# Performance work log

Measured on AMD Instinct MI355X. Metric: run time of the kernel, lower is better.

## Reference

```python
import jax, jax.numpy as jnp
import numpy as np

NUM_FUTURE = 4  # num_future_time_steps module constant


def _wmean(x, src, dst, ew, n):
    # Weighted mean aggregation over incoming edges (PyG SAGEConv aggr='mean'
    # with edge-weighted messages). x: [N,F] or [T,N,F].
    if x.ndim == 2:
        msg = x[src] * ew[:, None]                          # [E,F]
        agg = jax.ops.segment_sum(msg, dst, num_segments=n)  # [N,F]
    else:
        msg = x[:, src, :] * ew[None, :, None]              # [T,E,F]
        agg = jax.ops.segment_sum(jnp.moveaxis(msg, 1, 0), dst, num_segments=n)
        agg = jnp.moveaxis(agg, 0, 1)                       # [T,N,F]
    deg = jax.ops.segment_sum(jnp.ones_like(ew), dst, num_segments=n)
    return agg / jnp.clip(deg, 1.0)[:, None]


def _sage(x, src, dst, ew, Wr, Wroot, b, n):
    # WeightedSAGEConv: lin_rel(weighted-mean of neighbors) + lin_root(x)
    return _wmean(x, src, dst, ew, n) @ Wr + x @ Wroot + b


def _glstm(xseq, src, dst, ew, Wr, Wroot, b, h0, c0, n):
    # Graph LSTM: all four gates are WeightedSAGEConv([x_t, h]) ; the gate
    # convs share one gather/scatter (linear in agg), weights stacked to 4H.
    def step(carry, xt):
        h, c = carry
        inp = jnp.concatenate([xt, h], axis=-1)             # [N,2H]
        gates = _wmean(inp, src, dst, ew, n) @ Wr + inp @ Wroot + b  # [N,4H]
        i, f, g, o = jnp.split(gates, 4, axis=-1)
        c = jax.nn.sigmoid(f) * c + jax.nn.sigmoid(i) * jnp.tanh(g)
        h = jax.nn.sigmoid(o) * jnp.tanh(c)
        return (h, c), h
    (h, c), hs = jax.lax.scan(step, (h0, c0), xseq)
    return hs, c  # hs: [T,N,H]


def setup_inputs():
    T, N, E = 12, 20000, 400000
    F, H, O = 32, 64, 8
    key = jax.random.key(0)
    ks = jax.random.split(key, 12)
    nrm = lambda k, shp, fan: jax.random.normal(k, shp, dtype=jnp.float32) / np.float32(np.sqrt(fan))
    return {
        "x": jax.random.normal(ks[0], (T, N, F), dtype=jnp.float32),
        "edge_index": jax.random.randint(ks[1], (2, E), 0, N, dtype=jnp.int32),
        "edge_attr": jax.random.uniform(ks[2], (E,), dtype=jnp.float32),
        "sage_Wr": nrm(ks[3], (F, H), F),
        "sage_Wroot": nrm(ks[4], (F, H), F),
        "sage_b": jnp.zeros((H,), jnp.float32),
        "lstm1_Wr": nrm(ks[5], (2 * H, 4 * H), 2 * H),
        "lstm1_Wroot": nrm(ks[6], (2 * H, 4 * H), 2 * H),
        "lstm1_b": jnp.zeros((4 * H,), jnp.float32),
        "lstm2_Wr": nrm(ks[7], (2 * H, 4 * H), 2 * H),
        "lstm2_Wroot": nrm(ks[8], (2 * H, 4 * H), 2 * H),
        "lstm2_b": jnp.zeros((4 * H,), jnp.float32),
        "W_out": nrm(ks[9], (2 * H, O), 2 * H),
        "b_out": jnp.zeros((O,), jnp.float32),
    }


def reference(x, edge_index, edge_attr, sage_Wr, sage_Wroot, sage_b,
              lstm1_Wr, lstm1_Wroot, lstm1_b, lstm2_Wr, lstm2_Wroot, lstm2_b,
              W_out, b_out):
    src, dst = edge_index[0], edge_index[1]
    N = x.shape[1]
    H = sage_Wr.shape[1]
    emb = _sage(x, src, dst, edge_attr, sage_Wr, sage_Wroot, sage_b, N)  # [T,N,H]
    xr = jax.nn.relu(emb)  # dropout = identity (eval mode)
    h0 = jnp.zeros((N, H), x.dtype)
    c0 = jnp.zeros((N, H), x.dtype)
    h1, c1 = _glstm(xr, src, dst, edge_attr, lstm1_Wr, lstm1_Wroot, lstm1_b, h0, c0, N)
    h2, c2 = _glstm(xr, src, dst, edge_attr, lstm2_Wr, lstm2_Wroot, lstm2_b, h1[-1], c1, N)
    xs = jnp.concatenate([xr, h2], axis=-1)              # skip connection, [T,N,2H]
    out = xs[-NUM_FUTURE:] @ W_out + b_out               # [4,N,O]
    return out, c2, emb
```

## Files before the change

### kernel.cpp

```cpp
#include <hip/hip_runtime.h>
#include <math.h>

#define TT 12
#define FF 32
#define HH 64
#define OO 8
#define GG 256
#define NF 4
#define BR 16

typedef __bf16 bf16x8 __attribute__((ext_vector_type(8)));
typedef float  f32x4  __attribute__((ext_vector_type(4)));

__device__ __forceinline__ float sigmoidf_(float x){ return 1.f/(1.f+expf(-x)); }
__device__ __forceinline__ unsigned short f2bf(float f){
  unsigned int u = __float_as_uint(f);
  u += 0x7FFFu + ((u >> 16) & 1u);
  return (unsigned short)(u >> 16);
}
__device__ __forceinline__ float bf2f(unsigned short b){
  return __uint_as_float(((unsigned int)b) << 16);
}

__global__ void hist_kernel(const int* __restrict__ dst, int* __restrict__ cnt, int E){
  int e = blockIdx.x*blockDim.x + threadIdx.x;
  if (e < E) atomicAdd(&cnt[dst[e]], 1);
}

__global__ __launch_bounds__(1024) void scan_kernel(const int* __restrict__ cnt,
                                                    int* __restrict__ ptr,
                                                    float* __restrict__ invd, int N){
  __shared__ int buf[1024];
  __shared__ int carry;
  if (threadIdx.x == 0) carry = 0;
  __syncthreads();
  for (int base = 0; base < N; base += 1024){
    int i = base + threadIdx.x;
    int v = (i < N) ? cnt[i] : 0;
    buf[threadIdx.x] = v;
    __syncthreads();
    for (int off = 1; off < 1024; off <<= 1){
      int t = (threadIdx.x >= off) ? buf[threadIdx.x - off] : 0;
      __syncthreads();
      buf[threadIdx.x] += t;
      __syncthreads();
    }
    int incl = buf[threadIdx.x];
    if (i < N){
      ptr[i] = carry + incl - v;
      invd[i] = 1.f / fmaxf((float)v, 1.f);
    }
    __syncthreads();
    if (threadIdx.x == 1023){
      carry += incl;
      if (base + 1024 >= N) ptr[N] = carry;
    }
    __syncthreads();
  }
}

__global__ void fill_kernel(const int* __restrict__ src, const int* __restrict__ dst,
                            const float* __restrict__ ew, const int* __restrict__ ptr,
                            int* __restrict__ fill, int2* __restrict__ csr_sw, int E){
  int e = blockIdx.x*blockDim.x + threadIdx.x;
  if (e >= E) return;
  int d = dst[e];
  int pos = ptr[d] + atomicAdd(&fill[d], 1);
  int2 m; m.x = src[e]; m.y = __float_as_int(ew[e]);
  csr_sw[pos] = m;
}

__global__ void bf16_conv(const float* __restrict__ in, unsigned short* __restrict__ out, int n){
  int i = blockIdx.x*blockDim.x + threadIdx.x;
  if (i < n) out[i] = f2bf(in[i]);
}

__global__ void pack_wfrag(const float* __restrict__ Wr, const float* __restrict__ Wroot,
                           unsigned short* __restrict__ Wfrag){
  int idx = blockIdx.x*256 + threadIdx.x;
  if (idx >= 16*8*64*8) return;
  int e  = idx & 7;
  int l  = (idx >> 3) & 63;
  int ks = (idx >> 9) & 7;
  int jt = idx >> 12;
  int k = ks*32 + (l>>4)*8 + e;
  int j = jt*16 + (l&15);
  float v = (k < 128) ? Wr[(size_t)k*GG + j] : Wroot[(size_t)(k-128)*GG + j];
  Wfrag[idx] = f2bf(v);
}

__global__ void pack_sfrag(const float* __restrict__ Wr, const float* __restrict__ Wroot,
                           unsigned short* __restrict__ Sfrag){
  int idx = blockIdx.x*256 + threadIdx.x;
  if (idx >= 4*2*64*8) return;
  int e  = idx & 7;
  int l  = (idx >> 3) & 63;
  int ks = (idx >> 9) & 1;
  int jt = idx >> 10;
  int k = ks*32 + (l>>4)*8 + e;
  int j = jt*16 + (l&15);
  float v = (k < 32) ? Wr[(size_t)k*HH + j] : Wroot[(size_t)(k-32)*HH + j];
  Sfrag[idx] = f2bf(v);
}

__global__ __launch_bounds__(256) void sage_gather(
    const unsigned short* __restrict__ xb, const int* __restrict__ ptr,
    const int2* __restrict__ csr_sw,
    const float* __restrict__ invd, unsigned short* __restrict__ aggb, int N){
  int wave = threadIdx.x >> 6, lane = threadIdx.x & 63;
  int f = lane & 31, tp = lane >> 5;
  int n = blockIdx.x*4 + wave;
  if (n >= N) return;
  int beg = ptr[n], end = ptr[n+1];
  float id = invd[n];
  float acc[TT/2];
  #pragma unroll
  for (int th = 0; th < TT/2; ++th) acc[th] = 0.f;
  const size_t plane = (size_t)N*FF;
  int e = beg;
  for (; e+4 <= end; e += 4){
    int2 m0 = csr_sw[e], m1 = csr_sw[e+1], m2 = csr_sw[e+2], m3 = csr_sw[e+3];
    const unsigned short* p0 = xb + (size_t)m0.x*FF + f + (size_t)tp*plane;
    const unsigned short* p1 = xb + (size_t)m1.x*FF + f + (size_t)tp*plane;
    const unsigned short* p2 = xb + (size_t)m2.x*FF + f + (size_t)tp*plane;
    const unsigned short* p3 = xb + (size_t)m3.x*FF + f + (size_t)tp*plane;
    float w0 = __int_as_float(m0.y), w1 = __int_as_float(m1.y);
    float w2 = __int_as_float(m2.y), w3 = __int_as_float(m3.y);
    #pragma unroll
    for (int th = 0; th < TT/2; ++th)
      acc[th] += bf2f(p0[2*th*plane])*w0 + bf2f(p1[2*th*plane])*w1
               + bf2f(p2[2*th*plane])*w2 + bf2f(p3[2*th*plane])*w3;
  }
  for (; e < end; ++e){
    int2 m = csr_sw[e];
    const unsigned short* p = xb + (size_t)m.x*FF + f + (size_t)tp*plane;
    float wv = __int_as_float(m.y);
    #pragma unroll
    for (int th = 0; th < TT/2; ++th)
      acc[th] += bf2f(p[2*th*plane])*wv;
  }
  #pragma unroll
  for (int th = 0; th < TT/2; ++th)
    aggb[(size_t)(2*th+tp)*plane + (size_t)n*FF + f] = f2bf(acc[th] * id);
}

__global__ __launch_bounds__(256) void sage_mfma(
    const unsigned short* __restrict__ aggb, const unsigned short* __restrict__ xb,
    const unsigned short* __restrict__ Sfrag, const float* __restrict__ bias,
    float* __restrict__ emb, unsigned short* __restrict__ xrb, int Mrows){
  int tid = threadIdx.x, wave = tid >> 6, lane = tid & 63;
  int rbase = blockIdx.x*64 + wave*16;
  if (rbase >= Mrows) return;
  int l15 = lane & 15, l4 = lane >> 4;
  int row = rbase + l15;
  bf16x8 af0 = *(const bf16x8*)&aggb[(size_t)row*FF + l4*8];
  bf16x8 af1 = *(const bf16x8*)&xb  [(size_t)row*FF + l4*8];
  f32x4 acc[4];
  #pragma unroll
  for (int jt = 0; jt < 4; ++jt){
    float bv = bias[jt*16 + l15];
    acc[jt][0]=bv; acc[jt][1]=bv; acc[jt][2]=bv; acc[jt][3]=bv;
  }
  #pragma unroll
  for (int jt = 0; jt < 4; ++jt){
    bf16x8 b0 = *(const bf16x8*)&Sfrag[(size_t)(((jt*2+0)*64) + lane) * 8];
    bf16x8 b1 = *(const bf16x8*)&Sfrag[(size_t)(((jt*2+1)*64) + lane) * 8];
    acc[jt] = __builtin_amdgcn_mfma_f32_16x16x32_bf16(af0, b0, acc[jt], 0, 0, 0);
    acc[jt] = __builtin_amdgcn_mfma_f32_16x16x32_bf16(af1, b1, acc[jt], 0, 0, 0);
  }
  #pragma unroll
  for (int jt = 0; jt < 4; ++jt){
    int col = jt*16 + l15;
    #pragma unroll
    for (int i = 0; i < 4; ++i){
      int ro = rbase + l4*4 + i;
      float v = acc[jt][i];
      emb[(size_t)ro*HH + col] = v;
      xrb[(size_t)ro*HH + col] = f2bf(fmaxf(v, 0.f));
    }
  }
}

__global__ __launch_bounds__(256) void xr_gather(
    const unsigned short* __restrict__ xrb, const int* __restrict__ ptr,
    const int2* __restrict__ csr_sw,
    const float* __restrict__ invd, unsigned short* __restrict__ xr_aggb, int N){
  int wave = threadIdx.x >> 6, lane = threadIdx.x & 63;
  int n = blockIdx.x*4 + wave;
  if (n >= N) return;
  int beg = ptr[n], end = ptr[n+1];
  float id = invd[n];
  float acc[TT];
  #pragma unroll
  for (int t = 0; t < TT; ++t) acc[t] = 0.f;
  const size_t plane = (size_t)N*HH;
  int e = beg;
  for (; e+4 <= end; e += 4){
    int2 m0 = csr_sw[e], m1 = csr_sw[e+1], m2 = csr_sw[e+2], m3 = csr_sw[e+3];
    const unsigned short* p0 = xrb + (size_t)m0.x*HH + lane;
    const unsigned short* p1 = xrb + (size_t)m1.x*HH + lane;
    const unsigned short* p2 = xrb + (size_t)m2.x*HH + lane;
    const unsigned short* p3 = xrb + (size_t)m3.x*HH + lane;
    float w0 = __int_as_float(m0.y), w1 = __int_as_float(m1.y);
    float w2 = __int_as_float(m2.y), w3 = __int_as_float(m3.y);
    #pragma unroll
    for (int t = 0; t < TT; ++t)
      acc[t] += bf2f(p0[t*plane])*w0 + bf2f(p1[t*plane])*w1
              + bf2f(p2[t*plane])*w2 + bf2f(p3[t*plane])*w3;
  }
  for (; e < end; ++e){
    int2 m = csr_sw[e];
    const unsigned short* p = xrb + (size_t)m.x*HH + lane;
    float wv = __int_as_float(m.y);
    #pragma unroll
    for (int t = 0; t < TT; ++t)
      acc[t] += bf2f(p[t*plane])*wv;
  }
  #pragma unroll
  for (int t = 0; t < TT; ++t)
    xr_aggb[(size_t)t*plane + (size_t)n*HH + lane] = f2bf(acc[t] * id);
}

__global__ __launch_bounds__(1024) void lstm_mfma(
    const unsigned short* __restrict__ xrb_t, const unsigned short* __restrict__ xraggb_t,
    const unsigned short* __restrict__ h_prev, unsigned short* __restrict__ h_next,
    float* __restrict__ c, const float* __restrict__ invd,
    const int* __restrict__ ptr, const int2* __restrict__ csr_sw,
    const unsigned short* __restrict__ Wfrag, const float* __restrict__ bias,
    unsigned short* __restrict__ h2_store, int N){
  __shared__ __align__(16) unsigned short Albuf[BR][264];
  __shared__ float gbuf[BR][260];
  int tid = threadIdx.x, wave = tid >> 6, lane = tid & 63;
  int base = blockIdx.x * BR;
  int n = base + wave;

  if (n < N){
    float id = invd[n];
    int beg = ptr[n], end = ptr[n+1];
    float a0=0.f,a1=0.f,a2=0.f,a3=0.f,a4=0.f,a5=0.f,a6=0.f,a7=0.f;
    int e = beg;
    for (; e+8 <= end; e += 8){
      int2 m0=csr_sw[e+0], m1=csr_sw[e+1], m2=csr_sw[e+2], m3=csr_sw[e+3];
      int2 m4=csr_sw[e+4], m5=csr_sw[e+5], m6=csr_sw[e+6], m7=csr_sw[e+7];
      a0 += bf2f(h_prev[(size_t)m0.x*HH+lane])*__int_as_float(m0.y);
      a1 += bf2f(h_prev[(size_t)m1.x*HH+lane])*__int_as_float(m1.y);
      a2 += bf2f(h_prev[(size_t)m2.x*HH+lane])*__int_as_float(m2.y);
      a3 += bf2f(h_prev[(size_t)m3.x*HH+lane])*__int_as_float(m3.y);
      a4 += bf2f(h_prev[(size_t)m4.x*HH+lane])*__int_as_float(m4.y);
      a5 += bf2f(h_prev[(size_t)m5.x*HH+lane])*__int_as_float(m5.y);
      a6 += bf2f(h_prev[(size_t)m6.x*HH+lane])*__int_as_float(m6.y);
      a7 += bf2f(h_prev[(size_t)m7.x*HH+lane])*__int_as_float(m7.y);
    }
    for (; e < end; ++e){
      int2 m = csr_sw[e];
      a0 += bf2f(h_prev[(size_t)m.x*HH+lane])*__int_as_float(m.y);
    }
    float hag = (((a0+a1)+(a2+a3))+((a4+a5)+(a6+a7))) * id;
    Albuf[wave][    lane] = xraggb_t[(size_t)n*HH + lane];
    Albuf[wave][ 64+lane] = f2bf(hag);
    Albuf[wave][128+lane] = xrb_t [(size_t)n*HH + lane];
    Albuf[wave][192+lane] = h_prev[(size_t)n*HH + lane];
  } else {
    Albuf[wave][lane] = Albuf[wave][64+lane] = Albuf[wave][128+lane] = Albuf[wave][192+lane] = 0;
  }
  __syncthreads();

  int l15 = lane & 15, l4 = lane >> 4;
  int jt = wave;
  f32x4 acc;
  {
    float bv = bias[jt*16 + l15];
    acc[0]=bv; acc[1]=bv; acc[2]=bv; acc[3]=bv;
  }
  #pragma unroll
  for (int ks = 0; ks < 8; ++ks){
    bf16x8 af = *(const bf16x8*)&Albuf[l15][ks*32 + l4*8];
    bf16x8 bf = *(const bf16x8*)&Wfrag[(size_t)(((jt*8 + ks)*64) + lane) * 8];
    acc = __builtin_amdgcn_mfma_f32_16x16x32_bf16(af, bf, acc, 0, 0, 0);
  }
  {
    int col = jt*16 + l15;
    #pragma unroll
    for (int i = 0; i < 4; ++i)
      gbuf[l4*4 + i][col] = acc[i];
  }
  __syncthreads();

  if (n < N){
    int r = wave;
    float gi = gbuf[r][lane], gf = gbuf[r][64+lane], gg2 = gbuf[r][128+lane], go = gbuf[r][192+lane];
    float cn = sigmoidf_(gf)*c[(size_t)n*HH+lane] + sigmoidf_(gi)*tanhf(gg2);
    float hn = sigmoidf_(go)*tanhf(cn);
    c[(size_t)n*HH+lane] = cn;
    unsigned short hb = f2bf(hn);
    h_next[(size_t)n*HH+lane] = hb;
    if (h2_store) h2_store[(size_t)n*HH+lane] = hb;
  }
}

__global__ void out_gemm(const unsigned short* __restrict__ xr8, const unsigned short* __restrict__ h2s,
                         const float* __restrict__ Wout, const float* __restrict__ bout,
                         float* __restrict__ out, int N){
  int idx = blockIdx.x*blockDim.x + threadIdx.x;
  if (idx >= NF*N*OO) return;
  int o = idx & (OO-1);
  int row = idx >> 3;
  const unsigned short* xv = xr8 + (size_t)row*HH;
  const unsigned short* hv = h2s + (size_t)row*HH;
  float acc = bout[o];
  #pragma unroll
  for (int k = 0; k < HH; ++k)
    acc += bf2f(xv[k])*Wout[k*OO+o] + bf2f(hv[k])*Wout[(HH+k)*OO+o];
  out[idx] = acc;
}

__global__ void copyk(const float* __restrict__ s, float* __restrict__ d, int n){
  int i = blockIdx.x*blockDim.x + threadIdx.x;
  if (i < n) d[i] = s[i];
}

extern "C" void kernel_launch(void* const* d_in, const int* in_sizes, int n_in,
                              void* d_out, int out_size, void* d_ws, size_t ws_size,
                              hipStream_t stream){
  const float* x      = (const float*)d_in[0];
  const int*   ei     = (const int*)  d_in[1];
  const float* ew     = (const float*)d_in[2];
  const float* sWr    = (const float*)d_in[3];
  const float* sWroot = (const float*)d_in[4];
  const float* sb     = (const float*)d_in[5];
  const float* l1Wr   = (const float*)d_in[6];
  const float* l1Wroot= (const float*)d_in[7];
  const float* l1b    = (const float*)d_in[8];
  const float* l2Wr   = (const float*)d_in[9];
  const float* l2Wroot= (const float*)d_in[10];
  const float* l2b    = (const float*)d_in[11];
  const float* Wout   = (const float*)d_in[12];
  const float* bout   = (const float*)d_in[13];

  const int E = in_sizes[2];
  const int N = in_sizes[0] / (TT*FF);
  const int* src = ei;
  const int* dst = ei + E;

  float* out0   = (float*)d_out;
  float* c2out  = out0 + (size_t)NF*N*OO;
  float* embout = c2out + (size_t)N*HH;

  float* w = (float*)d_ws;
  float* cbuf   = w;  w += (size_t)N*HH;
  float* invd   = w;  w += N;
  int*   cnt    = (int*)w;  w += N;
  int*   fill   = (int*)w;  w += N;
  int*   ptr    = (int*)w;  w += (N+2);
  int2*  csr_sw = (int2*)w; w += (size_t)2*E;
  unsigned short* Wf1 = (unsigned short*)w; w += (size_t)16*8*64*8/2;
  unsigned short* Wf2 = (unsigned short*)w; w += (size_t)16*8*64*8/2;
  unsigned short* Sfg = (unsigned short*)w; w += (size_t)4*2*64*8/2;
  unsigned short* xb     = (unsigned short*)w; w += (size_t)TT*N*FF/2;
  unsigned short* aggb   = (unsigned short*)w; w += (size_t)TT*N*FF/2;
  unsigned short* xrb    = (unsigned short*)w; w += (size_t)TT*N*HH/2;
  unsigned short* xraggb = (unsigned short*)w; w += (size_t)TT*N*HH/2;
  unsigned short* hA     = (unsigned short*)w; w += (size_t)N*HH/2;
  unsigned short* hB     = (unsigned short*)w; w += (size_t)N*HH/2;
  unsigned short* h2s    = (unsigned short*)w; w += (size_t)NF*N*HH/2;

  hipMemsetAsync(cnt,  0, (size_t)N*4, stream);
  hipMemsetAsync(fill, 0, (size_t)N*4, stream);
  hipMemsetAsync(hA,   0, (size_t)N*HH*2, stream);
  hipMemsetAsync(cbuf, 0, (size_t)N*HH*4, stream);

  hist_kernel<<<(E+255)/256, 256, 0, stream>>>(dst, cnt, E);
  scan_kernel<<<1, 1024, 0, stream>>>(cnt, ptr, invd, N);
  fill_kernel<<<(E+255)/256, 256, 0, stream>>>(src, dst, ew, ptr, fill, csr_sw, E);

  pack_wfrag<<<(16*8*64*8+255)/256, 256, 0, stream>>>(l1Wr, l1Wroot, Wf1);
  pack_wfrag<<<(16*8*64*8+255)/256, 256, 0, stream>>>(l2Wr, l2Wroot, Wf2);
  pack_sfrag<<<(4*2*64*8+255)/256, 256, 0, stream>>>(sWr, sWroot, Sfg);
  bf16_conv<<<((size_t)TT*N*FF+255)/256, 256, 0, stream>>>(x, xb, TT*N*FF);

  sage_gather<<<(N+3)/4, 256, 0, stream>>>(xb, ptr, csr_sw, invd, aggb, N);
  {
    int Mrows = TT*N;
    sage_mfma<<<(Mrows+63)/64, 256, 0, stream>>>(aggb, xb, Sfg, sb, embout, xrb, Mrows);
  }
  xr_gather<<<(N+3)/4, 256, 0, stream>>>(xrb, ptr, csr_sw, invd, xraggb, N);

  const int sBlocks = (N+BR-1)/BR;
  unsigned short* hp = hA; unsigned short* hn = hB;
  for (int t = 0; t < TT; ++t){
    lstm_mfma<<<sBlocks, 1024, 0, stream>>>(xrb + (size_t)t*N*HH, xraggb + (size_t)t*N*HH,
                                            hp, hn, cbuf, invd, ptr, csr_sw,
                                            Wf1, l1b, nullptr, N);
    unsigned short* tmp = hp; hp = hn; hn = tmp;
  }
  for (int t = 0; t < TT; ++t){
    unsigned short* store = (t >= TT-NF) ? (h2s + (size_t)(t-(TT-NF))*N*HH) : nullptr;
    lstm_mfma<<<sBlocks, 1024, 0, stream>>>(xrb + (size_t)t*N*HH, xraggb + (size_t)t*N*HH,
                                            hp, hn, cbuf, invd, ptr, csr_sw,
                                            Wf2, l2b, store, N);
    unsigned short* tmp = hp; hp = hn; hn = tmp;
  }

  out_gemm<<<((size_t)NF*N*OO+255)/256, 256, 0, stream>>>(xrb + (size_t)(TT-NF)*N*HH, h2s,
                                                          Wout, bout, out0, N);
  copyk<<<((size_t)N*HH+255)/256, 256, 0, stream>>>(cbuf, c2out, N*HH);
}
```

Baseline: 1.115 ms.

## Store time-major activations node-major so gathers read contiguous per-neighbor rows

The bf16 copies of x, the relu'd embedding and the neighbor aggregates now use a [N,T,F] layout instead of [T,N,F]. A neighbor's full time series is then one contiguous block, so the sage and xr gathers touch fewer cache lines per edge. The unroll over edges drops from 4 to 2, and the LSTM steps index with a TT*HH stride. The conversion kernel now transposes, the emb output is scattered back to [T,N,H], and the LSTM reads of xrb/xraggb become strided per step.

```diff
diff --git a/kernel.cpp b/kernel.cpp
--- a/kernel.cpp
+++ b/kernel.cpp
@@ -70,9 +70,14 @@
   csr_sw[pos] = m;
 }
 
-__global__ void bf16_conv(const float* __restrict__ in, unsigned short* __restrict__ out, int n){
-  int i = blockIdx.x*blockDim.x + threadIdx.x;
-  if (i < n) out[i] = f2bf(in[i]);
+__global__ void xpose_conv(const float* __restrict__ in, unsigned short* __restrict__ out,
+                           int N){
+  int idx = blockIdx.x*blockDim.x + threadIdx.x;
+  if (idx >= TT*N*FF) return;
+  int f = idx & (FF-1);
+  int rem = idx >> 5;
+  int t = rem % TT, n = rem / TT;
+  out[idx] = f2bf(in[(size_t)t*N*FF + (size_t)n*FF + f]);
 }
 
 __global__ void pack_wfrag(const float* __restrict__ Wr, const float* __restrict__ Wroot,
@@ -116,38 +121,33 @@
   float acc[TT/2];
   #pragma unroll
   for (int th = 0; th < TT/2; ++th) acc[th] = 0.f;
-  const size_t plane = (size_t)N*FF;
   int e = beg;
-  for (; e+4 <= end; e += 4){
-    int2 m0 = csr_sw[e], m1 = csr_sw[e+1], m2 = csr_sw[e+2], m3 = csr_sw[e+3];
-    const unsigned short* p0 = xb + (size_t)m0.x*FF + f + (size_t)tp*plane;
-    const unsigned short* p1 = xb + (size_t)m1.x*FF + f + (size_t)tp*plane;
-    const unsigned short* p2 = xb + (size_t)m2.x*FF + f + (size_t)tp*plane;
-    const unsigned short* p3 = xb + (size_t)m3.x*FF + f + (size_t)tp*plane;
+  for (; e+2 <= end; e += 2){
+    int2 m0 = csr_sw[e], m1 = csr_sw[e+1];
+    const unsigned short* p0 = xb + (size_t)m0.x*TT*FF + tp*FF + f;
+    const unsigned short* p1 = xb + (size_t)m1.x*TT*FF + tp*FF + f;
     float w0 = __int_as_float(m0.y), w1 = __int_as_float(m1.y);
-    float w2 = __int_as_float(m2.y), w3 = __int_as_float(m3.y);
     #pragma unroll
     for (int th = 0; th < TT/2; ++th)
-      acc[th] += bf2f(p0[2*th*plane])*w0 + bf2f(p1[2*th*plane])*w1
-               + bf2f(p2[2*th*plane])*w2 + bf2f(p3[2*th*plane])*w3;
+      acc[th] += bf2f(p0[2*th*FF])*w0 + bf2f(p1[2*th*FF])*w1;
   }
   for (; e < end; ++e){
     int2 m = csr_sw[e];
-    const unsigned short* p = xb + (size_t)m.x*FF + f + (size_t)tp*plane;
+    const unsigned short* p = xb + (size_t)m.x*TT*FF + tp*FF + f;
     float wv = __int_as_float(m.y);
     #pragma unroll
     for (int th = 0; th < TT/2; ++th)
-      acc[th] += bf2f(p[2*th*plane])*wv;
+      acc[th] += bf2f(p[2*th*FF])*wv;
   }
   #pragma unroll
   for (int th = 0; th < TT/2; ++th)
-    aggb[(size_t)(2*th+tp)*plane + (size_t)n*FF + f] = f2bf(acc[th] * id);
+    aggb[(size_t)n*TT*FF + (2*th+tp)*FF + f] = f2bf(acc[th] * id);
 }
 
 __global__ __launch_bounds__(256) void sage_mfma(
     const unsigned short* __restrict__ aggb, const unsigned short* __restrict__ xb,
     const unsigned short* __restrict__ Sfrag, const float* __restrict__ bias,
-    float* __restrict__ emb, unsigned short* __restrict__ xrb, int Mrows){
+    float* __restrict__ emb, unsigned short* __restrict__ xrb, int N, int Mrows){
   int tid = threadIdx.x, wave = tid >> 6, lane = tid & 63;
   int rbase = blockIdx.x*64 + wave*16;
   if (rbase >= Mrows) return;
@@ -174,8 +174,9 @@
     #pragma unroll
     for (int i = 0; i < 4; ++i){
       int ro = rbase + l4*4 + i;
+      int t = ro % TT, n = ro / TT;
       float v = acc[jt][i];
-      emb[(size_t)ro*HH + col] = v;
+      emb[(size_t)t*N*HH + (size_t)n*HH + col] = v;
       xrb[(size_t)ro*HH + col] = f2bf(fmaxf(v, 0.f));
     }
   }
@@ -193,32 +194,27 @@
   float acc[TT];
   #pragma unroll
   for (int t = 0; t < TT; ++t) acc[t] = 0.f;
-  const size_t plane = (size_t)N*HH;
   int e = beg;
-  for (; e+4 <= end; e += 4){
-    int2 m0 = csr_sw[e], m1 = csr_sw[e+1], m2 = csr_sw[e+2], m3 = csr_sw[e+3];
-    const unsigned short* p0 = xrb + (size_t)m0.x*HH + lane;
-    const unsigned short* p1 = xrb + (size_t)m1.x*HH + lane;
-    const unsigned short* p2 = xrb + (size_t)m2.x*HH + lane;
-    const unsigned short* p3 = xrb + (size_t)m3.x*HH + lane;
+  for (; e+2 <= end; e += 2){
+    int2 m0 = csr_sw[e], m1 = csr_sw[e+1];
+    const unsigned short* p0 = xrb + (size_t)m0.x*TT*HH + lane;
+    const unsigned short* p1 = xrb + (size_t)m1.x*TT*HH + lane;
     float w0 = __int_as_float(m0.y), w1 = __int_as_float(m1.y);
-    float w2 = __int_as_float(m2.y), w3 = __int_as_float(m3.y);
     #pragma unroll
     for (int t = 0; t < TT; ++t)
-      acc[t] += bf2f(p0[t*plane])*w0 + bf2f(p1[t*plane])*w1
-              + bf2f(p2[t*plane])*w2 + bf2f(p3[t*plane])*w3;
+      acc[t] += bf2f(p0[t*HH])*w0 + bf2f(p1[t*HH])*w1;
   }
   for (; e < end; ++e){
     int2 m = csr_sw[e];
-    const unsigned short* p = xrb + (size_t)m.x*HH + lane;
+    const unsigned short* p = xrb + (size_t)m.x*TT*HH + lane;
     float wv = __int_as_float(m.y);
     #pragma unroll
     for (int t = 0; t < TT; ++t)
-      acc[t] += bf2f(p[t*plane])*wv;
+      acc[t] += bf2f(p[t*HH])*wv;
   }
   #pragma unroll
   for (int t = 0; t < TT; ++t)
-    xr_aggb[(size_t)t*plane + (size_t)n*HH + lane] = f2bf(acc[t] * id);
+    xr_aggb[(size_t)n*TT*HH + t*HH + lane] = f2bf(acc[t] * id);
 }
 
 __global__ __launch_bounds__(1024) void lstm_mfma(
@@ -256,9 +252,9 @@
       a0 += bf2f(h_prev[(size_t)m.x*HH+lane])*__int_as_float(m.y);
     }
     float hag = (((a0+a1)+(a2+a3))+((a4+a5)+(a6+a7))) * id;
-    Albuf[wave][    lane] = xraggb_t[(size_t)n*HH + lane];
+    Albuf[wave][    lane] = xraggb_t[(size_t)n*TT*HH + lane];
     Albuf[wave][ 64+lane] = f2bf(hag);
-    Albuf[wave][128+lane] = xrb_t [(size_t)n*HH + lane];
+    Albuf[wave][128+lane] = xrb_t [(size_t)n*TT*HH + lane];
     Albuf[wave][192+lane] = h_prev[(size_t)n*HH + lane];
   } else {
     Albuf[wave][lane] = Albuf[wave][64+lane] = Albuf[wave][128+lane] = Albuf[wave][192+lane] = 0;
@@ -298,14 +294,15 @@
   }
 }
 
-__global__ void out_gemm(const unsigned short* __restrict__ xr8, const unsigned short* __restrict__ h2s,
+__global__ void out_gemm(const unsigned short* __restrict__ xrb, const unsigned short* __restrict__ h2s,
                          const float* __restrict__ Wout, const float* __restrict__ bout,
                          float* __restrict__ out, int N){
   int idx = blockIdx.x*blockDim.x + threadIdx.x;
   if (idx >= NF*N*OO) return;
   int o = idx & (OO-1);
   int row = idx >> 3;
-  const unsigned short* xv = xr8 + (size_t)row*HH;
+  int tt = row / N, n = row % N;
+  const unsigned short* xv = xrb + ((size_t)n*TT + (TT-NF) + tt)*HH;
   const unsigned short* hv = h2s + (size_t)row*HH;
   float acc = bout[o];
   #pragma unroll
@@ -376,32 +373,32 @@
   pack_wfrag<<<(16*8*64*8+255)/256, 256, 0, stream>>>(l1Wr, l1Wroot, Wf1);
   pack_wfrag<<<(16*8*64*8+255)/256, 256, 0, stream>>>(l2Wr, l2Wroot, Wf2);
   pack_sfrag<<<(4*2*64*8+255)/256, 256, 0, stream>>>(sWr, sWroot, Sfg);
-  bf16_conv<<<((size_t)TT*N*FF+255)/256, 256, 0, stream>>>(x, xb, TT*N*FF);
+  xpose_conv<<<((size_t)TT*N*FF+255)/256, 256, 0, stream>>>(x, xb, N);
 
   sage_gather<<<(N+3)/4, 256, 0, stream>>>(xb, ptr, csr_sw, invd, aggb, N);
   {
     int Mrows = TT*N;
-    sage_mfma<<<(Mrows+63)/64, 256, 0, stream>>>(aggb, xb, Sfg, sb, embout, xrb, Mrows);
+    sage_mfma<<<(Mrows+63)/64, 256, 0, stream>>>(aggb, xb, Sfg, sb, embout, xrb, N, Mrows);
   }
   xr_gather<<<(N+3)/4, 256, 0, stream>>>(xrb, ptr, csr_sw, invd, xraggb, N);
 
   const int sBlocks = (N+BR-1)/BR;
   unsigned short* hp = hA; unsigned short* hn = hB;
   for (int t = 0; t < TT; ++t){
-    lstm_mfma<<<sBlocks, 1024, 0, stream>>>(xrb + (size_t)t*N*HH, xraggb + (size_t)t*N*HH,
+    lstm_mfma<<<sBlocks, 1024, 0, stream>>>(xrb + (size_t)t*HH, xraggb + (size_t)t*HH,
                                             hp, hn, cbuf, invd, ptr, csr_sw,
                                             Wf1, l1b, nullptr, N);
     unsigned short* tmp = hp; hp = hn; hn = tmp;
   }
   for (int t = 0; t < TT; ++t){
     unsigned short* store = (t >= TT-NF) ? (h2s + (size_t)(t-(TT-NF))*N*HH) : nullptr;
-    lstm_mfma<<<sBlocks, 1024, 0, stream>>>(xrb + (size_t)t*N*HH, xraggb + (size_t)t*N*HH,
+    lstm_mfma<<<sBlocks, 1024, 0, stream>>>(xrb + (size_t)t*HH, xraggb + (size_t)t*HH,
                                             hp, hn, cbuf, invd, ptr, csr_sw,
                                             Wf2, l2b, store, N);
     unsigned short* tmp = hp; hp = hn; hn = tmp;
   }
 
-  out_gemm<<<((size_t)NF*N*OO+255)/256, 256, 0, stream>>>(xrb + (size_t)(TT-NF)*N*HH, h2s,
+  out_gemm<<<((size_t)NF*N*OO+255)/256, 256, 0, stream>>>(xrb, h2s,
                                                           Wout, bout, out0, N);
   copyk<<<((size_t)N*HH+255)/256, 256, 0, stream>>>(cbuf, c2out, N*HH);
 }
```

Measured after the change: 1.004 ms. 9.9% less time.
